# Optimization experiments

Hardware: AMD Instinct MI355X
Metric: run time of the kernel (lower is better)

The kernel has to match this reference:

```python
import jax, jax.numpy as jnp
import numpy as np

D = 768   # embedding_dimensions (richness) — hardcoded in source
H = 3     # heads — hardcoded in source


def setup_inputs() -> dict:
    key = jax.random.key(0)
    ks = jax.random.split(key, 12)
    s = 1.0 / np.sqrt(D)
    s3 = 1.0 / np.sqrt(H * D)
    return {
        "x": jax.random.normal(ks[0], (4, 2048, D), dtype=jnp.float32),
        # QKV projections: Linear(D, D*H), stored as (in, out)
        "Wq": jax.random.uniform(ks[1], (D, D * H), jnp.float32, -s, s),
        "bq": jax.random.uniform(ks[2], (D * H,), jnp.float32, -s, s),
        "Wk": jax.random.uniform(ks[3], (D, D * H), jnp.float32, -s, s),
        "bk": jax.random.uniform(ks[4], (D * H,), jnp.float32, -s, s),
        "Wv": jax.random.uniform(ks[5], (D, D * H), jnp.float32, -s, s),
        "bv": jax.random.uniform(ks[6], (D * H,), jnp.float32, -s, s),
        # final projection: Linear(H*D, D)
        "Wo": jax.random.uniform(ks[7], (H * D, D), jnp.float32, -s3, s3),
        "bo": jax.random.uniform(ks[8], (D,), jnp.float32, -s3, s3),
        # FFN: Linear(D, D) + LeakyReLU
        "Wf": jax.random.uniform(ks[9], (D, D), jnp.float32, -s, s),
        "bf": jax.random.uniform(ks[10], (D,), jnp.float32, -s, s),
    }


def reference(x, Wq, bq, Wk, bk, Wv, bv, Wo, bo, Wf, bf):
    B, S, _ = x.shape
    # QKV: [B,S,H*D] -> [B,H,S,D]  (head dim == full D, as in source)
    q = (x @ Wq + bq).reshape(B, S, H, D).transpose(0, 2, 1, 3)
    k = (x @ Wk + bk).reshape(B, S, H, D).transpose(0, 2, 1, 3)
    v = (x @ Wv + bv).reshape(B, S, H, D).transpose(0, 2, 1, 3)
    # unscaled attention scores (source applies no 1/sqrt(d))
    scores = jnp.einsum('bhqd,bhkd->bhqk', q, k)
    # faithful masking: tril of the scores themselves, fill zeros with -99999
    masked = jnp.where(jnp.tril(scores) == 0, jnp.float32(-99999.0), scores)
    attn = jax.nn.softmax(masked, axis=-1)
    o = jnp.einsum('bhqk,bhkd->bhqd', attn, v)
    o = o.transpose(0, 2, 1, 3).reshape(B, S, H * D)
    a = o @ Wo + bo
    # "normalisation": subtract global mean over the whole tensor
    n = a - jnp.mean(a)
    y = n + x  # residual
    return jax.nn.leaky_relu(y @ Wf + bf, negative_slope=0.01)
```

## Files before the change

kernel.cpp:

```cpp
#include <hip/hip_runtime.h>
#include <hip/hip_bf16.h>

typedef __attribute__((ext_vector_type(8))) __bf16 bf16x8;
typedef __attribute__((ext_vector_type(4))) float f32x4;
typedef unsigned short u16;

#define DEV static __device__ __forceinline__

#define BAR() asm volatile("s_barrier" ::: "memory")
#define VMCNT3() asm volatile("s_waitcnt vmcnt(3)" ::: "memory")
#define VMCNT0() asm volatile("s_waitcnt vmcnt(0)" ::: "memory")

DEV void load_lds16(const void* g, void* l) {
  __builtin_amdgcn_global_load_lds(
      (const __attribute__((address_space(1))) unsigned int*)g,
      (__attribute__((address_space(3))) unsigned int*)l, 16, 0, 0);
}

DEV u16 bf16bits(float v) {
  __hip_bfloat16 h = __float2bfloat16(v);
  return __builtin_bit_cast(u16, h);
}

DEV float bf2f(u16 u) {
  return __builtin_bit_cast(float, (unsigned)u << 16);
}

DEV bf16x8 rdfrag(const u16* region, int row, int ks, int l) {
  const int cb = (((ks << 6) | ((l >> 4) << 4)) ^ ((l & 7) << 4));
  return *(const bf16x8*)((const char*)region + row * 128 + cb);
}

DEV bf16x8 rdfrag32(const u16* region, int row, int l) {
  const int cb = (((l >> 4) ^ ((row >> 1) & 3)) << 4);
  return *(const bf16x8*)((const char*)region + row * 64 + cb);
}

struct OffN { unsigned long long a[12], b[12], c[12]; };

enum { G128_SC = 0, G128_PV = 1, G128_PLAIN = 2, G128_LEAKY = 3 };

__global__ __launch_bounds__(512, 1) void k_qkv256(
    const u16* __restrict__ A, const u16* __restrict__ B,
    const float* __restrict__ bias, u16* __restrict__ C, u16* __restrict__ Vt)
{
  int flat = blockIdx.y * 27 + blockIdx.x;
  flat = (flat & 7) * 108 + (flat >> 3);
  const int n0 = (flat % 27) * 256, m0 = (flat / 27) * 256;
  const int lda = 768, ldb = 768, nkt = 12;

  __shared__ u16 smem[65536];

  const int tid = threadIdx.x;
  const int l = tid & 63;
  const int wid = tid >> 6;
  const int wm = wid >> 1, wn = wid & 1;

  const int r0s = wid * 16 + (l >> 3);
  const int ces = ((l & 7) ^ (l >> 3)) << 3;
  const size_t aR0 = (size_t)(m0 + r0s) * lda + ces;
  const size_t aR1 = aR0 + (size_t)8 * lda;
  const size_t bR0 = (size_t)(n0 + r0s) * ldb + ces;
  const size_t bR1 = bR0 + (size_t)8 * ldb;
  const size_t hA = (size_t)128 * lda, hB = (size_t)128 * ldb;
  const int dst0 = wid * 1024 + l * 8, dst1 = dst0 + 512;
  u16* As0 = smem;
  u16* Bs0 = smem + 32768;

#define STAGE_A(bf, h, kkv) do {                                 \
    u16* Lp = As0 + (bf) * 16384 + (h) * 8192;                   \
    load_lds16(A + aR0 + ((h) ? hA : 0) + (kkv), Lp + dst0);     \
    load_lds16(A + aR1 + ((h) ? hA : 0) + (kkv), Lp + dst1);     \
  } while (0)
#define STAGE_B(bf, h, kkv) do {                                 \
    u16* Lp = Bs0 + (bf) * 16384 + (h) * 8192;                   \
    load_lds16(B + bR0 + ((h) ? hB : 0) + (kkv), Lp + dst0);     \
    load_lds16(B + bR1 + ((h) ? hB : 0) + (kkv), Lp + dst1);     \
  } while (0)

  f32x4 acc[2][2][2][4] = {};
  bf16x8 af[2][2], bA[4][2], bB[4][2];

#define MFMA16(QM, QN, BARR)                                                  \
    __builtin_amdgcn_s_setprio(1);                                            \
    _Pragma("unroll") for (int ks = 0; ks < 2; ks++)                          \
      _Pragma("unroll") for (int fm = 0; fm < 2; fm++)                        \
        _Pragma("unroll") for (int fn = 0; fn < 4; fn++)                      \
          acc[QM][QN][fm][fn] = __builtin_amdgcn_mfma_f32_16x16x32_bf16(      \
              af[fm][ks], BARR[fn][ks], acc[QM][QN][fm][fn], 0, 0, 0);        \
    __builtin_amdgcn_s_setprio(0);

#define RD_A(half)                                                            \
    _Pragma("unroll") for (int fm = 0; fm < 2; fm++)                          \
      _Pragma("unroll") for (int ks = 0; ks < 2; ks++)                        \
        af[fm][ks] = rdfrag(half, wm * 32 + fm * 16 + (l & 15), ks, l);
#define RD_B(dstv, half)                                                      \
    _Pragma("unroll") for (int fn = 0; fn < 4; fn++)                          \
      _Pragma("unroll") for (int ks = 0; ks < 2; ks++)                        \
        dstv[fn][ks] = rdfrag(half, wn * 64 + fn * 16 + (l & 15), ks, l);

  STAGE_A(0, 0, 0); STAGE_B(0, 0, 0); STAGE_B(0, 1, 0); STAGE_A(0, 1, 0);
  STAGE_A(1, 0, 64); STAGE_B(1, 0, 64); STAGE_B(1, 1, 64);
  VMCNT3();
  BAR();

  for (int t = 0; t < nkt; ++t) {
    const int cur = t & 1, nxt = cur ^ 1;
    const int kk1 = (t + 1) << 6, kk2 = (t + 2) << 6;
    const bool s1 = (t + 1 < nkt), s2 = (t + 2 < nkt);
    RD_A(As0 + cur * 16384);
    RD_B(bA, Bs0 + cur * 16384);
    if (s1) STAGE_A(nxt, 1, kk1);
    BAR();
    MFMA16(0, 0, bA);
    BAR();
    RD_B(bB, Bs0 + cur * 16384 + 8192);
    if (s2) STAGE_A(cur, 0, kk2);
    BAR();
    MFMA16(0, 1, bB);
    BAR();
    RD_A(As0 + cur * 16384 + 8192);
    if (s2) STAGE_B(cur, 0, kk2);
    BAR();
    MFMA16(1, 1, bB);
    BAR();
    if (s2) STAGE_B(cur, 1, kk2);
    BAR();
    MFMA16(1, 0, bA);
    if (s2) { VMCNT3(); } else { VMCNT0(); }
    BAR();
  }
#undef RD_A
#undef RD_B
#undef MFMA16
#undef STAGE_A
#undef STAGE_B

  __syncthreads();
  const int sel = n0 >= 4608 ? 2 : (n0 >= 2304 ? 1 : 0);
  const int r0c = (l >> 4) << 2;
  if (sel == 2) {
#pragma unroll
    for (int Qm = 0; Qm < 2; Qm++)
#pragma unroll
      for (int Qn = 0; Qn < 2; Qn++)
#pragma unroll
        for (int fn = 0; fn < 4; fn++) {
          const int coll = Qn * 128 + wn * 64 + fn * 16 + (l & 15);
          const float bv = bias[n0 + coll];
#pragma unroll
          for (int fm = 0; fm < 2; fm++)
#pragma unroll
            for (int r = 0; r < 4; r++) {
              const int rowl = Qm * 128 + wm * 32 + fm * 16 + r0c + r;
              smem[coll * 256 + ((((rowl >> 3) ^ (coll & 7)) << 3) | (rowl & 7))] =
                  bf16bits(acc[Qm][Qn][fm][fn][r] + bv);
            }
        }
    __syncthreads();
    const int n0v = n0 - 4608;
    const int h = n0v / 768, d0l = n0v % 768;
    const int b = m0 >> 11, sbase = m0 & 2047;
    u16* Cb = Vt + ((size_t)(b * 3 + h) * 768 + d0l) * 2048 + sbase;
#pragma unroll
    for (int j = 0; j < 16; j++) {
      const int dr = j * 16 + (tid >> 5);
      const int c8 = tid & 31;
      bf16x8 v = *(const bf16x8*)&smem[dr * 256 + ((c8 ^ (dr & 7)) << 3)];
      *(bf16x8*)&Cb[(size_t)dr * 2048 + c8 * 8] = v;
    }
  } else {
#pragma unroll
    for (int Qm = 0; Qm < 2; Qm++)
#pragma unroll
      for (int Qn = 0; Qn < 2; Qn++)
#pragma unroll
        for (int fn = 0; fn < 4; fn++) {
          const int coll = Qn * 128 + wn * 64 + fn * 16 + (l & 15);
          const float bv = bias[n0 + coll];
#pragma unroll
          for (int fm = 0; fm < 2; fm++)
#pragma unroll
            for (int r = 0; r < 4; r++) {
              const int rowl = Qm * 128 + wm * 32 + fm * 16 + r0c + r;
              smem[rowl * 256 + (coll ^ (((rowl >> 2) & 3) << 4))] =
                  bf16bits(acc[Qm][Qn][fm][fn][r] + bv);
            }
        }
    __syncthreads();
    u16* Cb = C + (size_t)sel * (8192ull * 2304) + (n0 - sel * 2304);
#pragma unroll
    for (int j = 0; j < 16; j++) {
      const int rowl = j * 16 + (tid >> 5);
      const int c = (tid & 31) * 8;
      bf16x8 v = *(const bf16x8*)&smem[rowl * 256 + (c ^ (((rowl >> 2) & 3) << 4))];
      *(bf16x8*)&Cb[(size_t)(m0 + rowl) * 2304 + c] = v;
    }
  }
}

template<int MODE>
__global__ __launch_bounds__(512, 4) void k_g128(
    const u16* __restrict__ Abase, const u16* __restrict__ Bbase,
    const float* __restrict__ bias, void* __restrict__ Cbase,
    float* __restrict__ part,
    long lda, long ldb, long ldc, int K, OffN off)
{
  int m0, n0, z, r = 0, rb = 0, nkt, arow0, brow0;
  const u16 *A, *B;
  if (MODE == G128_SC) {
    r = blockIdx.y; z = blockIdx.z;
    rb = r >> 1;
    if ((int)blockIdx.x > rb) return;
    m0 = r * 128; n0 = blockIdx.x * 256;
    nkt = K >> 5;
    A = Abase + off.a[z]; B = Bbase + off.b[z];
    arow0 = m0; brow0 = n0;
  } else if (MODE == G128_PV) {
    r = 15 - (int)blockIdx.y;
    rb = r >> 1;
    z = blockIdx.x / 3;
    m0 = r * 128; n0 = (blockIdx.x % 3) * 256;
    nkt = (rb + 1) * 8;
    lda = (long)(rb + 1) * 256;
    A = Abase + off.a[z] + (size_t)32768 * rb * (rb + 1);
    B = Bbase + off.b[z];
    arow0 = (r & 1) * 128; brow0 = n0;
  } else {
    z = 0;
    m0 = blockIdx.y * 128; n0 = blockIdx.x * 256;
    nkt = K >> 5;
    A = Abase; B = Bbase;
    arow0 = m0; brow0 = n0;
  }

  __shared__ u16 smem[36864];

  const int tid = threadIdx.x;
  const int l = tid & 63;
  const int wid = tid >> 6;
  const int wm = wid & 1;
  const int wn = wid >> 1;

  const int ces = (((tid & 3) ^ ((tid >> 3) & 3)) << 3);
  const u16* aS  = A + (size_t)(arow0 + (tid >> 2)) * lda + ces;
  const u16* bS0 = B + (size_t)(brow0 + (tid >> 2)) * ldb + ces;
  const u16* bS1 = bS0 + (size_t)128 * ldb;
  const int t8 = tid * 8;

#define STG(buf, kkv) do {                         \
    u16* Lp = smem + (buf) * 12288;                \
    load_lds16(aS + (kkv), Lp + t8);               \
    load_lds16(bS0 + (kkv), Lp + 4096 + t8);       \
    load_lds16(bS1 + (kkv), Lp + 8192 + t8);       \
  } while (0)

  f32x4 acc[4][4] = {};
  bf16x8 af[4], bf[4];

  STG(0, 0);
  STG(1, 32);
  VMCNT3();
  BAR();

  for (int t = 0; t < nkt; ++t) {
    const u16* Ar = smem + (t % 3) * 12288;
    const u16* Br = Ar + 4096;
#pragma unroll
    for (int fm = 0; fm < 4; fm++)
      af[fm] = rdfrag32(Ar, wm * 64 + fm * 16 + (l & 15), l);
#pragma unroll
    for (int fn = 0; fn < 4; fn++)
      bf[fn] = rdfrag32(Br, wn * 64 + fn * 16 + (l & 15), l);
    const bool s2 = (t + 2 < nkt);
    if (s2) STG((t + 2) % 3, (t + 2) << 5);
    __builtin_amdgcn_s_setprio(1);
#pragma unroll
    for (int fm = 0; fm < 4; fm++)
#pragma unroll
      for (int fn = 0; fn < 4; fn++)
        acc[fm][fn] = __builtin_amdgcn_mfma_f32_16x16x32_bf16(
            af[fm], bf[fn], acc[fm][fn], 0, 0, 0);
    __builtin_amdgcn_s_setprio(0);
    if (s2) { VMCNT3(); } else if (t + 1 < nkt) { VMCNT0(); }
    BAR();
  }
#undef STG

  const int r0c = (l >> 4) << 2;
  if (MODE == G128_SC) {
    float mx4[4][4], s4[4][4];
#pragma unroll
    for (int fm = 0; fm < 4; fm++)
#pragma unroll
      for (int rr = 0; rr < 4; rr++) {
        const int gi = m0 + wm * 64 + fm * 16 + r0c + rr;
        float mv = -1e30f;
#pragma unroll
        for (int fn = 0; fn < 4; fn++) {
          const int gc = n0 + wn * 64 + fn * 16 + (l & 15);
          float v = (gc <= gi) ? acc[fm][fn][rr] : -1e30f;
          acc[fm][fn][rr] = v;
          mv = fmaxf(mv, v);
        }
        mx4[fm][rr] = mv;
      }
#pragma unroll
    for (int o = 1; o < 16; o <<= 1)
#pragma unroll
      for (int fm = 0; fm < 4; fm++)
#pragma unroll
        for (int rr = 0; rr < 4; rr++)
          mx4[fm][rr] = fmaxf(mx4[fm][rr], __shfl_xor(mx4[fm][rr], o, 64));
    float* redm = (float*)smem;
    float* reds = redm + 512;
#pragma unroll
    for (int fm = 0; fm < 4; fm++)
#pragma unroll
      for (int rr = 0; rr < 4; rr++)
        if ((l & 15) == fm * 4 + rr)
          redm[(wm * 64 + fm * 16 + r0c + rr) * 4 + wn] = mx4[fm][rr];
    __syncthreads();
#pragma unroll
    for (int fm = 0; fm < 4; fm++)
#pragma unroll
      for (int rr = 0; rr < 4; rr++) {
        const int rowl = wm * 64 + fm * 16 + r0c + rr;
        f32x4 rm = *(const f32x4*)&redm[rowl * 4];
        const float tm = fmaxf(fmaxf(rm[0], rm[1]), fmaxf(rm[2], rm[3]));
        float ss = 0.f;
#pragma unroll
        for (int fn = 0; fn < 4; fn++) {
          const float e = __expf(acc[fm][fn][rr] - tm);
          acc[fm][fn][rr] = e;
          ss += e;
        }
        s4[fm][rr] = ss;
      }
#pragma unroll
    for (int o = 1; o < 16; o <<= 1)
#pragma unroll
      for (int fm = 0; fm < 4; fm++)
#pragma unroll
        for (int rr = 0; rr < 4; rr++)
          s4[fm][rr] += __shfl_xor(s4[fm][rr], o, 64);
#pragma unroll
    for (int fm = 0; fm < 4; fm++)
#pragma unroll
      for (int rr = 0; rr < 4; rr++)
        if ((l & 15) == fm * 4 + rr)
          reds[(wm * 64 + fm * 16 + r0c + rr) * 4 + wn] = s4[fm][rr];
    __syncthreads();
    if (tid < 128) {
      f32x4 rm = *(const f32x4*)&redm[tid * 4];
      f32x4 rs = *(const f32x4*)&reds[tid * 4];
      float2 pw;
      pw.x = fmaxf(fmaxf(rm[0], rm[1]), fmaxf(rm[2], rm[3]));
      pw.y = rs[0] + rs[1] + rs[2] + rs[3];
      ((float2*)part)[((size_t)z * 8 + blockIdx.x) * 2048 + m0 + tid] = pw;
    }
    __syncthreads();
#pragma unroll
    for (int fn = 0; fn < 4; fn++) {
      const int coll = wn * 64 + fn * 16 + (l & 15);
#pragma unroll
      for (int fm = 0; fm < 4; fm++)
#pragma unroll
        for (int rr = 0; rr < 4; rr++) {
          const int rowl = wm * 64 + fm * 16 + r0c + rr;
          smem[rowl * 256 + (coll ^ (((rowl >> 2) & 3) << 4))] =
              bf16bits(acc[fm][fn][rr]);
        }
    }
    __syncthreads();
    u16* Cb = (u16*)Cbase + off.c[z] + (size_t)32768 * rb * (rb + 1);
    const int W = (rb + 1) << 8;
    const int pr0 = (r & 1) * 128;
#pragma unroll
    for (int j = 0; j < 8; j++) {
      const int rowl = j * 16 + (tid >> 5);
      const int c = (tid & 31) * 8;
      bf16x8 v = *(const bf16x8*)&smem[rowl * 256 + (c ^ (((rowl >> 2) & 3) << 4))];
      *(bf16x8*)&Cb[(size_t)(pr0 + rowl) * W + n0 + c] = v;
    }
  } else if (MODE == G128_PV) {
    __syncthreads();
#pragma unroll
    for (int fn = 0; fn < 4; fn++) {
      const int coll = wn * 64 + fn * 16 + (l & 15);
#pragma unroll
      for (int fm = 0; fm < 4; fm++)
#pragma unroll
        for (int rr = 0; rr < 4; rr++) {
          const int rowl = wm * 64 + fm * 16 + r0c + rr;
          smem[rowl * 256 + (coll ^ (((rowl >> 2) & 3) << 4))] =
              bf16bits(acc[fm][fn][rr]);
        }
    }
    __syncthreads();
    u16* Cb = (u16*)Cbase + off.c[z] + n0;
#pragma unroll
    for (int j = 0; j < 8; j++) {
      const int rowl = j * 16 + (tid >> 5);
      const int c = (tid & 31) * 8;
      bf16x8 v = *(const bf16x8*)&smem[rowl * 256 + (c ^ (((rowl >> 2) & 3) << 4))];
      *(bf16x8*)&Cb[(size_t)(m0 + rowl) * 2304 + c] = v;
    }
  } else {
#pragma unroll
    for (int fn = 0; fn < 4; fn++) {
      const int col = n0 + wn * 64 + fn * 16 + (l & 15);
      const float bv = bias[col];
#pragma unroll
      for (int fm = 0; fm < 4; fm++)
#pragma unroll
        for (int rr = 0; rr < 4; rr++) {
          const int rowl = wm * 64 + fm * 16 + r0c + rr;
          float v = acc[fm][fn][rr] + bv;
          if (MODE == G128_LEAKY) v = v > 0.f ? v : 0.01f * v;
          ((float*)Cbase)[(size_t)(m0 + rowl) * ldc + col] = v;
        }
    }
  }
}

__global__ __launch_bounds__(256) void k_cast_x(const float* __restrict__ in,
                                                u16* __restrict__ out) {
  const size_t i = ((size_t)blockIdx.x * 256 + threadIdx.x) * 4;
  float4 v = *(const float4*)&in[i];
  ushort4 o;
  o.x = bf16bits(v.x); o.y = bf16bits(v.y); o.z = bf16bits(v.z); o.w = bf16bits(v.w);
  *(ushort4*)&out[i] = o;
}

__global__ __launch_bounds__(256) void k_wt(const float* __restrict__ in,
                                            u16* __restrict__ out, int R, int C) {
  __shared__ float tile[32][33];
  const int c0 = blockIdx.x * 32, r0 = blockIdx.y * 32;
  const int tx = threadIdx.x, ty = threadIdx.y;
#pragma unroll
  for (int k = 0; k < 4; k++)
    tile[ty + 8 * k][tx] = in[(size_t)(r0 + ty + 8 * k) * C + c0 + tx];
  __syncthreads();
#pragma unroll
  for (int k = 0; k < 4; k++)
    out[(size_t)(c0 + ty + 8 * k) * R + r0 + tx] = bf16bits(tile[tx][ty + 8 * k]);
}

__global__ __launch_bounds__(256) void k_bias_concat(const float* __restrict__ bq,
                                                     const float* __restrict__ bk,
                                                     const float* __restrict__ bv,
                                                     float* __restrict__ out) {
  const int i = blockIdx.x * 256 + threadIdx.x;
  if (i < 2304) out[i] = bq[i];
  else if (i < 4608) out[i] = bk[i - 2304];
  else if (i < 6912) out[i] = bv[i - 4608];
}

__global__ __launch_bounds__(256) void k_rescale(u16* __restrict__ P,
                                                 const float* __restrict__ part) {
  const int w = threadIdx.x >> 6, l = threadIdx.x & 63;
  const int gi = blockIdx.x * 4 + w;
  const int z = blockIdx.y;
  const int rb = gi >> 8;
  const int W = (rb + 1) << 8;
  const int nt = rb + 1;
  const float2* pp = (const float2*)part + (size_t)z * 16384 + gi;
  float m = -1e30f;
  for (int t = 0; t < nt; t++) m = fmaxf(m, pp[(size_t)t * 2048].x);
  float den = 0.f;
  for (int t = 0; t < nt; t++) {
    float2 q = pp[(size_t)t * 2048];
    den += q.y * __expf(q.x - m);
  }
  const float inv = 1.f / den;
  u16* Prow = P + (size_t)z * 2359296 + (size_t)32768 * rb * (rb + 1) +
              (size_t)(gi & 255) * W;
  for (int t = 0; t < nt; t++) {
    const float ft = __expf(pp[(size_t)t * 2048].x - m) * inv;
    ushort4 v = *(const ushort4*)&Prow[t * 256 + l * 4];
    v.x = bf16bits(bf2f(v.x) * ft);
    v.y = bf16bits(bf2f(v.y) * ft);
    v.z = bf16bits(bf2f(v.z) * ft);
    v.w = bf16bits(bf2f(v.w) * ft);
    *(ushort4*)&Prow[t * 256 + l * 4] = v;
  }
}

__global__ __launch_bounds__(256) void k_red1(const float* __restrict__ a,
                                              float* __restrict__ part) {
  float s = 0.f;
  for (size_t idx = (size_t)blockIdx.x * 256 + threadIdx.x; idx < 6291456ull; idx += 2048ull * 256)
    s += a[idx];
#pragma unroll
  for (int o = 32; o >= 1; o >>= 1) s += __shfl_xor(s, o, 64);
  __shared__ float r[4];
  const int t = threadIdx.x, w = t >> 6;
  if ((t & 63) == 0) r[w] = s;
  __syncthreads();
  if (t == 0) part[blockIdx.x] = r[0] + r[1] + r[2] + r[3];
}

__global__ __launch_bounds__(256) void k_red2(const float* __restrict__ part,
                                              float* __restrict__ mean) {
  const int t = threadIdx.x;
  float s = 0.f;
  for (int i = t; i < 2048; i += 256) s += part[i];
#pragma unroll
  for (int o = 32; o >= 1; o >>= 1) s += __shfl_xor(s, o, 64);
  __shared__ float r[4];
  const int w = t >> 6;
  if ((t & 63) == 0) r[w] = s;
  __syncthreads();
  if (t == 0) mean[0] = (r[0] + r[1] + r[2] + r[3]) * (1.f / 6291456.f);
}

__global__ __launch_bounds__(256) void k_residual(const float* __restrict__ a,
                                                  const float* __restrict__ x,
                                                  const float* __restrict__ meanp,
                                                  u16* __restrict__ yb) {
  const float mean = meanp[0];
  const size_t i = ((size_t)blockIdx.x * 256 + threadIdx.x) * 4;
  float4 av = *(const float4*)&a[i];
  float4 xv = *(const float4*)&x[i];
  ushort4 o;
  o.x = bf16bits(av.x - mean + xv.x);
  o.y = bf16bits(av.y - mean + xv.y);
  o.z = bf16bits(av.z - mean + xv.z);
  o.w = bf16bits(av.w - mean + xv.w);
  *(ushort4*)&yb[i] = o;
}

extern "C" void kernel_launch(void* const* d_in, const int* in_sizes, int n_in,
                              void* d_out, int out_size, void* d_ws, size_t ws_size,
                              hipStream_t stream) {
  const float* x   = (const float*)d_in[0];
  const float* Wq  = (const float*)d_in[1];
  const float* bq  = (const float*)d_in[2];
  const float* Wk  = (const float*)d_in[3];
  const float* bk  = (const float*)d_in[4];
  const float* Wv  = (const float*)d_in[5];
  const float* bv  = (const float*)d_in[6];
  const float* Wo  = (const float*)d_in[7];
  const float* bo  = (const float*)d_in[8];
  const float* Wf  = (const float*)d_in[9];
  const float* bfb = (const float*)d_in[10];

  char* ws = (char*)d_ws;
  const size_t MSZ    = 37748736;
  const size_t o_Wqkvt = 0;
  const size_t o_Wot  = 10616832;
  const size_t o_Wft  = o_Wot + 3538944;
  const size_t o_bqkv = o_Wft + 1179648;
  const size_t o_prt  = o_bqkv + 32768;
  const size_t o_mn   = o_prt + 8192;
  const size_t o_part = o_mn + 256;
  const size_t o_xb   = o_part + 1572864;
  const size_t o_Q    = o_xb + 12582912;
  const size_t o_K    = o_Q + MSZ;
  const size_t o_Vt   = o_K + MSZ;
  const size_t o_P    = o_Vt + MSZ;
  const size_t o_end  = o_P + 56623104;
  if (ws_size < o_end) return;

  const size_t o_O  = o_Q;
  const size_t o_a  = o_K;
  const size_t o_yb = o_xb;

  OffN z0{};
  dim3 b32(32, 8);

  k_cast_x<<<6144, 256, 0, stream>>>(x, (u16*)(ws + o_xb));
  k_wt<<<dim3(72, 24), b32, 0, stream>>>(Wq, (u16*)(ws + o_Wqkvt), 768, 2304);
  k_wt<<<dim3(72, 24), b32, 0, stream>>>(Wk, (u16*)(ws + o_Wqkvt) + 2304 * 768, 768, 2304);
  k_wt<<<dim3(72, 24), b32, 0, stream>>>(Wv, (u16*)(ws + o_Wqkvt) + 2 * 2304 * 768, 768, 2304);
  k_wt<<<dim3(24, 72), b32, 0, stream>>>(Wo, (u16*)(ws + o_Wot), 2304, 768);
  k_wt<<<dim3(24, 24), b32, 0, stream>>>(Wf, (u16*)(ws + o_Wft), 768, 768);
  k_bias_concat<<<27, 256, 0, stream>>>(bq, bk, bv, (float*)(ws + o_bqkv));

  k_qkv256<<<dim3(27, 32), 512, 0, stream>>>(
      (const u16*)(ws + o_xb), (const u16*)(ws + o_Wqkvt),
      (const float*)(ws + o_bqkv), (u16*)(ws + o_Q), (u16*)(ws + o_Vt));

  OffN so{}, po{};
  for (int zz = 0; zz < 12; zz++) {
    const int b = zz / 3, h = zz % 3;
    so.a[zz] = (size_t)b * 2048 * 2304 + (size_t)h * 768;
    so.b[zz] = so.a[zz];
    so.c[zz] = (size_t)zz * 2359296;
    po.a[zz] = so.c[zz];
    po.b[zz] = (size_t)zz * 768 * 2048;
    po.c[zz] = so.a[zz];
  }
  k_g128<G128_SC><<<dim3(8, 16, 12), 512, 0, stream>>>(
      (const u16*)(ws + o_Q), (const u16*)(ws + o_K), nullptr, ws + o_P,
      (float*)(ws + o_part), 2304, 2304, 0, 768, so);
  k_rescale<<<dim3(512, 12), 256, 0, stream>>>((u16*)(ws + o_P),
                                               (const float*)(ws + o_part));
  k_g128<G128_PV><<<dim3(36, 16), 512, 0, stream>>>(
      (const u16*)(ws + o_P), (const u16*)(ws + o_Vt), nullptr, ws + o_O,
      nullptr, 0, 2048, 0, 0, po);

  k_g128<G128_PLAIN><<<dim3(3, 64), 512, 0, stream>>>(
      (const u16*)(ws + o_O), (const u16*)(ws + o_Wot), bo, ws + o_a,
      nullptr, 2304, 2304, 768, 2304, z0);

  k_red1<<<2048, 256, 0, stream>>>((const float*)(ws + o_a), (float*)(ws + o_prt));
  k_red2<<<1, 256, 0, stream>>>((const float*)(ws + o_prt), (float*)(ws + o_mn));
  k_residual<<<6144, 256, 0, stream>>>((const float*)(ws + o_a), x,
                                       (const float*)(ws + o_mn), (u16*)(ws + o_yb));

  k_g128<G128_LEAKY><<<dim3(3, 64), 512, 0, stream>>>(
      (const u16*)(ws + o_yb), (const u16*)(ws + o_Wft), bfb, d_out,
      nullptr, 768, 768, 768, 768, z0);
}
```

Before: 387.4 us.

## Restructure QKV GEMM to triple-buffered K=32 pipeline and merge weight transposes

Rewrites the QKV GEMM main loop to use K-steps of 32 with a three-stage LDS ring buffer and one barrier per iteration, in place of the previous K=64 double-buffer with many interleaved barriers. LDS use drops to 96KB and launch bounds allow two blocks per CU to raise occupancy. The epilogue now writes out in two halves to fit the smaller LDS, which adds extra syncs. The three QKV weight-transpose launches are also merged into one 3D-grid launch to cut launch overhead.

```diff
diff --git a/kernel.cpp b/kernel.cpp
--- a/kernel.cpp
+++ b/kernel.cpp
@@ -8,6 +8,7 @@
 #define DEV static __device__ __forceinline__
 
 #define BAR() asm volatile("s_barrier" ::: "memory")
+#define VMCNT4() asm volatile("s_waitcnt vmcnt(4)" ::: "memory")
 #define VMCNT3() asm volatile("s_waitcnt vmcnt(3)" ::: "memory")
 #define VMCNT0() asm volatile("s_waitcnt vmcnt(0)" ::: "memory")
 
@@ -26,11 +27,6 @@
   return __builtin_bit_cast(float, (unsigned)u << 16);
 }
 
-DEV bf16x8 rdfrag(const u16* region, int row, int ks, int l) {
-  const int cb = (((ks << 6) | ((l >> 4) << 4)) ^ ((l & 7) << 4));
-  return *(const bf16x8*)((const char*)region + row * 128 + cb);
-}
-
 DEV bf16x8 rdfrag32(const u16* region, int row, int l) {
   const int cb = (((l >> 4) ^ ((row >> 1) & 3)) << 4);
   return *(const bf16x8*)((const char*)region + row * 64 + cb);
@@ -40,161 +36,131 @@
 
 enum { G128_SC = 0, G128_PV = 1, G128_PLAIN = 2, G128_LEAKY = 3 };
 
-__global__ __launch_bounds__(512, 1) void k_qkv256(
+__global__ __launch_bounds__(512, 2) void k_qkv256(
     const u16* __restrict__ A, const u16* __restrict__ B,
     const float* __restrict__ bias, u16* __restrict__ C, u16* __restrict__ Vt)
 {
   int flat = blockIdx.y * 27 + blockIdx.x;
   flat = (flat & 7) * 108 + (flat >> 3);
   const int n0 = (flat % 27) * 256, m0 = (flat / 27) * 256;
-  const int lda = 768, ldb = 768, nkt = 12;
-
-  __shared__ u16 smem[65536];
+  const int nkt = 24;
+
+  __shared__ u16 smem[49152];
 
   const int tid = threadIdx.x;
   const int l = tid & 63;
   const int wid = tid >> 6;
-  const int wm = wid >> 1, wn = wid & 1;
-
-  const int r0s = wid * 16 + (l >> 3);
-  const int ces = ((l & 7) ^ (l >> 3)) << 3;
-  const size_t aR0 = (size_t)(m0 + r0s) * lda + ces;
-  const size_t aR1 = aR0 + (size_t)8 * lda;
-  const size_t bR0 = (size_t)(n0 + r0s) * ldb + ces;
-  const size_t bR1 = bR0 + (size_t)8 * ldb;
-  const size_t hA = (size_t)128 * lda, hB = (size_t)128 * ldb;
-  const int dst0 = wid * 1024 + l * 8, dst1 = dst0 + 512;
-  u16* As0 = smem;
-  u16* Bs0 = smem + 32768;
-
-#define STAGE_A(bf, h, kkv) do {                                 \
-    u16* Lp = As0 + (bf) * 16384 + (h) * 8192;                   \
-    load_lds16(A + aR0 + ((h) ? hA : 0) + (kkv), Lp + dst0);     \
-    load_lds16(A + aR1 + ((h) ? hA : 0) + (kkv), Lp + dst1);     \
+  const int wm = wid >> 1;
+  const int wn = wid & 1;
+
+  const int ces = (((tid & 3) ^ ((tid >> 3) & 3)) << 3);
+  const u16* aS = A + (size_t)(m0 + (tid >> 2)) * 768 + ces;
+  const u16* bS = B + (size_t)(n0 + (tid >> 2)) * 768 + ces;
+  const int t8 = tid * 8;
+
+#define STG(buf, kkv) do {                               \
+    u16* Lp = smem + (buf) * 16384;                      \
+    load_lds16(aS + (kkv), Lp + t8);                     \
+    load_lds16(aS + 128 * 768 + (kkv), Lp + 4096 + t8);  \
+    load_lds16(bS + (kkv), Lp + 8192 + t8);              \
+    load_lds16(bS + 128 * 768 + (kkv), Lp + 12288 + t8); \
   } while (0)
-#define STAGE_B(bf, h, kkv) do {                                 \
-    u16* Lp = Bs0 + (bf) * 16384 + (h) * 8192;                   \
-    load_lds16(B + bR0 + ((h) ? hB : 0) + (kkv), Lp + dst0);     \
-    load_lds16(B + bR1 + ((h) ? hB : 0) + (kkv), Lp + dst1);     \
-  } while (0)
-
-  f32x4 acc[2][2][2][4] = {};
-  bf16x8 af[2][2], bA[4][2], bB[4][2];
-
-#define MFMA16(QM, QN, BARR)                                                  \
-    __builtin_amdgcn_s_setprio(1);                                            \
-    _Pragma("unroll") for (int ks = 0; ks < 2; ks++)                          \
-      _Pragma("unroll") for (int fm = 0; fm < 2; fm++)                        \
-        _Pragma("unroll") for (int fn = 0; fn < 4; fn++)                      \
-          acc[QM][QN][fm][fn] = __builtin_amdgcn_mfma_f32_16x16x32_bf16(      \
-              af[fm][ks], BARR[fn][ks], acc[QM][QN][fm][fn], 0, 0, 0);        \
+
+  f32x4 acc[4][8] = {};
+  bf16x8 af[4], bf[8];
+
+  STG(0, 0);
+  STG(1, 32);
+  VMCNT4();
+  BAR();
+
+  for (int t = 0; t < nkt; ++t) {
+    const u16* Ar = smem + (t % 3) * 16384;
+    const u16* Br = Ar + 8192;
+#pragma unroll
+    for (int fm = 0; fm < 4; fm++)
+      af[fm] = rdfrag32(Ar, wm * 64 + fm * 16 + (l & 15), l);
+#pragma unroll
+    for (int fn = 0; fn < 8; fn++)
+      bf[fn] = rdfrag32(Br, wn * 128 + fn * 16 + (l & 15), l);
+    const bool s2 = (t + 2 < nkt);
+    if (s2) STG((t + 2) % 3, (t + 2) << 5);
+    __builtin_amdgcn_s_setprio(1);
+#pragma unroll
+    for (int fm = 0; fm < 4; fm++)
+#pragma unroll
+      for (int fn = 0; fn < 8; fn++)
+        acc[fm][fn] = __builtin_amdgcn_mfma_f32_16x16x32_bf16(
+            af[fm], bf[fn], acc[fm][fn], 0, 0, 0);
     __builtin_amdgcn_s_setprio(0);
-
-#define RD_A(half)                                                            \
-    _Pragma("unroll") for (int fm = 0; fm < 2; fm++)                          \
-      _Pragma("unroll") for (int ks = 0; ks < 2; ks++)                        \
-        af[fm][ks] = rdfrag(half, wm * 32 + fm * 16 + (l & 15), ks, l);
-#define RD_B(dstv, half)                                                      \
-    _Pragma("unroll") for (int fn = 0; fn < 4; fn++)                          \
-      _Pragma("unroll") for (int ks = 0; ks < 2; ks++)                        \
-        dstv[fn][ks] = rdfrag(half, wn * 64 + fn * 16 + (l & 15), ks, l);
-
-  STAGE_A(0, 0, 0); STAGE_B(0, 0, 0); STAGE_B(0, 1, 0); STAGE_A(0, 1, 0);
-  STAGE_A(1, 0, 64); STAGE_B(1, 0, 64); STAGE_B(1, 1, 64);
-  VMCNT3();
-  BAR();
-
-  for (int t = 0; t < nkt; ++t) {
-    const int cur = t & 1, nxt = cur ^ 1;
-    const int kk1 = (t + 1) << 6, kk2 = (t + 2) << 6;
-    const bool s1 = (t + 1 < nkt), s2 = (t + 2 < nkt);
-    RD_A(As0 + cur * 16384);
-    RD_B(bA, Bs0 + cur * 16384);
-    if (s1) STAGE_A(nxt, 1, kk1);
+    if (s2) { VMCNT4(); } else if (t + 1 < nkt) { VMCNT0(); }
     BAR();
-    MFMA16(0, 0, bA);
-    BAR();
-    RD_B(bB, Bs0 + cur * 16384 + 8192);
-    if (s2) STAGE_A(cur, 0, kk2);
-    BAR();
-    MFMA16(0, 1, bB);
-    BAR();
-    RD_A(As0 + cur * 16384 + 8192);
-    if (s2) STAGE_B(cur, 0, kk2);
-    BAR();
-    MFMA16(1, 1, bB);
-    BAR();
-    if (s2) STAGE_B(cur, 1, kk2);
-    BAR();
-    MFMA16(1, 0, bA);
-    if (s2) { VMCNT3(); } else { VMCNT0(); }
-    BAR();
-  }
-#undef RD_A
-#undef RD_B
-#undef MFMA16
-#undef STAGE_A
-#undef STAGE_B
-
+  }
+#undef STG
+
+  const int r0c = (l >> 4) << 2;
+  const int sel = n0 >= 4608 ? 2 : (n0 >= 2304 ? 1 : 0);
   __syncthreads();
-  const int sel = n0 >= 4608 ? 2 : (n0 >= 2304 ? 1 : 0);
-  const int r0c = (l >> 4) << 2;
   if (sel == 2) {
-#pragma unroll
-    for (int Qm = 0; Qm < 2; Qm++)
-#pragma unroll
-      for (int Qn = 0; Qn < 2; Qn++)
-#pragma unroll
-        for (int fn = 0; fn < 4; fn++) {
-          const int coll = Qn * 128 + wn * 64 + fn * 16 + (l & 15);
+    const int n0v = n0 - 4608;
+    const int hh = n0v / 768, d0l = n0v % 768;
+    const int bb = m0 >> 11, sbase = m0 & 2047;
+    u16* Cb = Vt + ((size_t)(bb * 3 + hh) * 768 + d0l) * 2048 + sbase;
+#pragma unroll
+    for (int hc = 0; hc < 2; hc++) {
+      if (wn == hc) {
+#pragma unroll
+        for (int fn = 0; fn < 8; fn++) {
+          const int cl = fn * 16 + (l & 15);
+          const float bv = bias[n0 + hc * 128 + cl];
+#pragma unroll
+          for (int fm = 0; fm < 4; fm++)
+#pragma unroll
+            for (int rr = 0; rr < 4; rr++) {
+              const int rowl = wm * 64 + fm * 16 + r0c + rr;
+              smem[cl * 256 + ((((rowl >> 3) ^ (cl & 7)) << 3) | (rowl & 7))] =
+                  bf16bits(acc[fm][fn][rr] + bv);
+            }
+        }
+      }
+      __syncthreads();
+#pragma unroll
+      for (int j = 0; j < 8; j++) {
+        const int cl = j * 16 + (tid >> 5);
+        const int c8 = tid & 31;
+        bf16x8 v = *(const bf16x8*)&smem[cl * 256 + ((c8 ^ (cl & 7)) << 3)];
+        *(bf16x8*)&Cb[(size_t)(hc * 128 + cl) * 2048 + c8 * 8] = v;
+      }
+      __syncthreads();
+    }
+  } else {
+    u16* Cb = C + (size_t)sel * (8192ull * 2304) + (n0 - sel * 2304);
+#pragma unroll
+    for (int hf = 0; hf < 2; hf++) {
+      if ((wm >> 1) == hf) {
+#pragma unroll
+        for (int fn = 0; fn < 8; fn++) {
+          const int coll = wn * 128 + fn * 16 + (l & 15);
           const float bv = bias[n0 + coll];
 #pragma unroll
-          for (int fm = 0; fm < 2; fm++)
-#pragma unroll
-            for (int r = 0; r < 4; r++) {
-              const int rowl = Qm * 128 + wm * 32 + fm * 16 + r0c + r;
-              smem[coll * 256 + ((((rowl >> 3) ^ (coll & 7)) << 3) | (rowl & 7))] =
-                  bf16bits(acc[Qm][Qn][fm][fn][r] + bv);
+          for (int fm = 0; fm < 4; fm++)
+#pragma unroll
+            for (int rr = 0; rr < 4; rr++) {
+              const int rloc = (wm & 1) * 64 + fm * 16 + r0c + rr;
+              smem[rloc * 256 + (coll ^ (((rloc >> 2) & 3) << 4))] =
+                  bf16bits(acc[fm][fn][rr] + bv);
             }
         }
-    __syncthreads();
-    const int n0v = n0 - 4608;
-    const int h = n0v / 768, d0l = n0v % 768;
-    const int b = m0 >> 11, sbase = m0 & 2047;
-    u16* Cb = Vt + ((size_t)(b * 3 + h) * 768 + d0l) * 2048 + sbase;
-#pragma unroll
-    for (int j = 0; j < 16; j++) {
-      const int dr = j * 16 + (tid >> 5);
-      const int c8 = tid & 31;
-      bf16x8 v = *(const bf16x8*)&smem[dr * 256 + ((c8 ^ (dr & 7)) << 3)];
-      *(bf16x8*)&Cb[(size_t)dr * 2048 + c8 * 8] = v;
-    }
-  } else {
-#pragma unroll
-    for (int Qm = 0; Qm < 2; Qm++)
-#pragma unroll
-      for (int Qn = 0; Qn < 2; Qn++)
-#pragma unroll
-        for (int fn = 0; fn < 4; fn++) {
-          const int coll = Qn * 128 + wn * 64 + fn * 16 + (l & 15);
-          const float bv = bias[n0 + coll];
-#pragma unroll
-          for (int fm = 0; fm < 2; fm++)
-#pragma unroll
-            for (int r = 0; r < 4; r++) {
-              const int rowl = Qm * 128 + wm * 32 + fm * 16 + r0c + r;
-              smem[rowl * 256 + (coll ^ (((rowl >> 2) & 3) << 4))] =
-                  bf16bits(acc[Qm][Qn][fm][fn][r] + bv);
-            }
-        }
-    __syncthreads();
-    u16* Cb = C + (size_t)sel * (8192ull * 2304) + (n0 - sel * 2304);
-#pragma unroll
-    for (int j = 0; j < 16; j++) {
-      const int rowl = j * 16 + (tid >> 5);
-      const int c = (tid & 31) * 8;
-      bf16x8 v = *(const bf16x8*)&smem[rowl * 256 + (c ^ (((rowl >> 2) & 3) << 4))];
-      *(bf16x8*)&Cb[(size_t)(m0 + rowl) * 2304 + c] = v;
+      }
+      __syncthreads();
+#pragma unroll
+      for (int j = 0; j < 8; j++) {
+        const int rowl = j * 16 + (tid >> 5);
+        const int c = (tid & 31) * 8;
+        bf16x8 v = *(const bf16x8*)&smem[rowl * 256 + (c ^ (((rowl >> 2) & 3) << 4))];
+        *(bf16x8*)&Cb[(size_t)(m0 + hf * 128 + rowl) * 2304 + c] = v;
+      }
+      __syncthreads();
     }
   }
 }
@@ -433,6 +399,24 @@
   *(ushort4*)&out[i] = o;
 }
 
+__global__ __launch_bounds__(256) void k_wt3(const float* __restrict__ w0,
+                                             const float* __restrict__ w1,
+                                             const float* __restrict__ w2,
+                                             u16* __restrict__ out) {
+  const float* in = blockIdx.z == 0 ? w0 : (blockIdx.z == 1 ? w1 : w2);
+  u16* o = out + (size_t)blockIdx.z * 2304 * 768;
+  __shared__ float tile[32][33];
+  const int c0 = blockIdx.x * 32, r0 = blockIdx.y * 32;
+  const int tx = threadIdx.x, ty = threadIdx.y;
+#pragma unroll
+  for (int k = 0; k < 4; k++)
+    tile[ty + 8 * k][tx] = in[(size_t)(r0 + ty + 8 * k) * 2304 + c0 + tx];
+  __syncthreads();
+#pragma unroll
+  for (int k = 0; k < 4; k++)
+    o[(size_t)(c0 + ty + 8 * k) * 768 + r0 + tx] = bf16bits(tile[tx][ty + 8 * k]);
+}
+
 __global__ __launch_bounds__(256) void k_wt(const float* __restrict__ in,
                                             u16* __restrict__ out, int R, int C) {
   __shared__ float tile[32][33];
@@ -571,9 +555,7 @@
   dim3 b32(32, 8);
 
   k_cast_x<<<6144, 256, 0, stream>>>(x, (u16*)(ws + o_xb));
-  k_wt<<<dim3(72, 24), b32, 0, stream>>>(Wq, (u16*)(ws + o_Wqkvt), 768, 2304);
-  k_wt<<<dim3(72, 24), b32, 0, stream>>>(Wk, (u16*)(ws + o_Wqkvt) + 2304 * 768, 768, 2304);
-  k_wt<<<dim3(72, 24), b32, 0, stream>>>(Wv, (u16*)(ws + o_Wqkvt) + 2 * 2304 * 768, 768, 2304);
+  k_wt3<<<dim3(72, 24, 3), b32, 0, stream>>>(Wq, Wk, Wv, (u16*)(ws + o_Wqkvt));
   k_wt<<<dim3(24, 72), b32, 0, stream>>>(Wo, (u16*)(ws + o_Wot), 2304, 768);
   k_wt<<<dim3(24, 24), b32, 0, stream>>>(Wf, (u16*)(ws + o_Wft), 768, 768);
   k_bias_concat<<<27, 256, 0, stream>>>(bq, bk, bv, (float*)(ws + o_bqkv));
```

Measured after the change: 392.1 us. About the same (+1.2%).

## Fuse softmax rescale into PV GEMM and merge QKV weight transposes

Applied to the files above, without the earlier changes.

Removes the standalone k_rescale pass, which read and rewrote the whole bf16 probability matrix. Instead, the PV kernel computes per-row, per-block exp factors and the inverse denominator into an LDS table. It scales the A fragments in registers before each MFMA and applies 1/den in the epilogue. The three Q/K/V weight transposes now run as one launch, and the QKV GEMM's vmcnt wait is relaxed from 3 to 6 outstanding loads. The trade is extra VALU work and LDS reads inside the PV main loop. The looser vmcnt wait risks reading staged data before it has landed.

```diff
diff --git a/kernel.cpp b/kernel.cpp
--- a/kernel.cpp
+++ b/kernel.cpp
@@ -8,6 +8,8 @@
 #define DEV static __device__ __forceinline__
 
 #define BAR() asm volatile("s_barrier" ::: "memory")
+#define LGKM0() asm volatile("s_waitcnt lgkmcnt(0)" ::: "memory")
+#define VMCNT6() asm volatile("s_waitcnt vmcnt(6)" ::: "memory")
 #define VMCNT3() asm volatile("s_waitcnt vmcnt(3)" ::: "memory")
 #define VMCNT0() asm volatile("s_waitcnt vmcnt(0)" ::: "memory")
 
@@ -20,10 +22,6 @@
 DEV u16 bf16bits(float v) {
   __hip_bfloat16 h = __float2bfloat16(v);
   return __builtin_bit_cast(u16, h);
-}
-
-DEV float bf2f(u16 u) {
-  return __builtin_bit_cast(float, (unsigned)u << 16);
 }
 
 DEV bf16x8 rdfrag(const u16* region, int row, int ks, int l) {
@@ -101,7 +99,7 @@
 
   STAGE_A(0, 0, 0); STAGE_B(0, 0, 0); STAGE_B(0, 1, 0); STAGE_A(0, 1, 0);
   STAGE_A(1, 0, 64); STAGE_B(1, 0, 64); STAGE_B(1, 1, 64);
-  VMCNT3();
+  VMCNT6();
   BAR();
 
   for (int t = 0; t < nkt; ++t) {
@@ -127,7 +125,7 @@
     if (s2) STAGE_B(cur, 1, kk2);
     BAR();
     MFMA16(1, 0, bA);
-    if (s2) { VMCNT3(); } else { VMCNT0(); }
+    if (s2) { VMCNT6(); } else { VMCNT0(); }
     BAR();
   }
 #undef RD_A
@@ -234,7 +232,7 @@
     arow0 = m0; brow0 = n0;
   }
 
-  __shared__ u16 smem[36864];
+  __shared__ u16 smem[39168];
 
   const int tid = threadIdx.x;
   const int l = tid & 63;
@@ -255,6 +253,24 @@
     load_lds16(bS1 + (kkv), Lp + 8192 + t8);       \
   } while (0)
 
+  float* ftab = (float*)(smem + 36864);
+  if (MODE == G128_PV) {
+    if (tid < 128) {
+      const float2* pp = (const float2*)part + (size_t)z * 16384 + (m0 + tid);
+      float m = -1e30f;
+      for (int t = 0; t <= rb; t++) m = fmaxf(m, pp[(size_t)t * 2048].x);
+      float den = 0.f;
+      for (int t = 0; t <= rb; t++) {
+        const float2 q = pp[(size_t)t * 2048];
+        const float e = __expf(q.x - m);
+        den += q.y * e;
+        ftab[tid * 9 + t] = e;
+      }
+      ftab[tid * 9 + 8] = 1.f / den;
+    }
+    LGKM0();
+  }
+
   f32x4 acc[4][4] = {};
   bf16x8 af[4], bf[4];
 
@@ -272,6 +288,17 @@
 #pragma unroll
     for (int fn = 0; fn < 4; fn++)
       bf[fn] = rdfrag32(Br, wn * 64 + fn * 16 + (l & 15), l);
+    if (MODE == G128_PV) {
+      const int tcol = t >> 3;
+#pragma unroll
+      for (int fm = 0; fm < 4; fm++) {
+        const int row = wm * 64 + fm * 16 + (l & 15);
+        const float ft = ftab[row * 9 + tcol];
+#pragma unroll
+        for (int i = 0; i < 8; i++)
+          af[fm][i] = (__bf16)((float)af[fm][i] * ft);
+      }
+    }
     const bool s2 = (t + 2 < nkt);
     if (s2) STG((t + 2) % 3, (t + 2) << 5);
     __builtin_amdgcn_s_setprio(1);
@@ -394,7 +421,7 @@
         for (int rr = 0; rr < 4; rr++) {
           const int rowl = wm * 64 + fm * 16 + r0c + rr;
           smem[rowl * 256 + (coll ^ (((rowl >> 2) & 3) << 4))] =
-              bf16bits(acc[fm][fn][rr]);
+              bf16bits(acc[fm][fn][rr] * ftab[rowl * 9 + 8]);
         }
     }
     __syncthreads();
@@ -431,6 +458,24 @@
   ushort4 o;
   o.x = bf16bits(v.x); o.y = bf16bits(v.y); o.z = bf16bits(v.z); o.w = bf16bits(v.w);
   *(ushort4*)&out[i] = o;
+}
+
+__global__ __launch_bounds__(256) void k_wt3(const float* __restrict__ w0,
+                                             const float* __restrict__ w1,
+                                             const float* __restrict__ w2,
+                                             u16* __restrict__ out) {
+  const float* in = blockIdx.z == 0 ? w0 : (blockIdx.z == 1 ? w1 : w2);
+  u16* o = out + (size_t)blockIdx.z * 2304 * 768;
+  __shared__ float tile[32][33];
+  const int c0 = blockIdx.x * 32, r0 = blockIdx.y * 32;
+  const int tx = threadIdx.x, ty = threadIdx.y;
+#pragma unroll
+  for (int k = 0; k < 4; k++)
+    tile[ty + 8 * k][tx] = in[(size_t)(r0 + ty + 8 * k) * 2304 + c0 + tx];
+  __syncthreads();
+#pragma unroll
+  for (int k = 0; k < 4; k++)
+    o[(size_t)(c0 + ty + 8 * k) * 768 + r0 + tx] = bf16bits(tile[tx][ty + 8 * k]);
 }
 
 __global__ __launch_bounds__(256) void k_wt(const float* __restrict__ in,
@@ -455,36 +500,6 @@
   if (i < 2304) out[i] = bq[i];
   else if (i < 4608) out[i] = bk[i - 2304];
   else if (i < 6912) out[i] = bv[i - 4608];
-}
-
-__global__ __launch_bounds__(256) void k_rescale(u16* __restrict__ P,
-                                                 const float* __restrict__ part) {
-  const int w = threadIdx.x >> 6, l = threadIdx.x & 63;
-  const int gi = blockIdx.x * 4 + w;
-  const int z = blockIdx.y;
-  const int rb = gi >> 8;
-  const int W = (rb + 1) << 8;
-  const int nt = rb + 1;
-  const float2* pp = (const float2*)part + (size_t)z * 16384 + gi;
-  float m = -1e30f;
-  for (int t = 0; t < nt; t++) m = fmaxf(m, pp[(size_t)t * 2048].x);
-  float den = 0.f;
-  for (int t = 0; t < nt; t++) {
-    float2 q = pp[(size_t)t * 2048];
-    den += q.y * __expf(q.x - m);
-  }
-  const float inv = 1.f / den;
-  u16* Prow = P + (size_t)z * 2359296 + (size_t)32768 * rb * (rb + 1) +
-              (size_t)(gi & 255) * W;
-  for (int t = 0; t < nt; t++) {
-    const float ft = __expf(pp[(size_t)t * 2048].x - m) * inv;
-    ushort4 v = *(const ushort4*)&Prow[t * 256 + l * 4];
-    v.x = bf16bits(bf2f(v.x) * ft);
-    v.y = bf16bits(bf2f(v.y) * ft);
-    v.z = bf16bits(bf2f(v.z) * ft);
-    v.w = bf16bits(bf2f(v.w) * ft);
-    *(ushort4*)&Prow[t * 256 + l * 4] = v;
-  }
 }
 
 __global__ __launch_bounds__(256) void k_red1(const float* __restrict__ a,
@@ -571,9 +586,7 @@
   dim3 b32(32, 8);
 
   k_cast_x<<<6144, 256, 0, stream>>>(x, (u16*)(ws + o_xb));
-  k_wt<<<dim3(72, 24), b32, 0, stream>>>(Wq, (u16*)(ws + o_Wqkvt), 768, 2304);
-  k_wt<<<dim3(72, 24), b32, 0, stream>>>(Wk, (u16*)(ws + o_Wqkvt) + 2304 * 768, 768, 2304);
-  k_wt<<<dim3(72, 24), b32, 0, stream>>>(Wv, (u16*)(ws + o_Wqkvt) + 2 * 2304 * 768, 768, 2304);
+  k_wt3<<<dim3(72, 24, 3), b32, 0, stream>>>(Wq, Wk, Wv, (u16*)(ws + o_Wqkvt));
   k_wt<<<dim3(24, 72), b32, 0, stream>>>(Wo, (u16*)(ws + o_Wot), 2304, 768);
   k_wt<<<dim3(24, 24), b32, 0, stream>>>(Wf, (u16*)(ws + o_Wft), 768, 768);
   k_bias_concat<<<27, 256, 0, stream>>>(bq, bk, bv, (float*)(ws + o_bqkv));
@@ -595,11 +608,9 @@
   k_g128<G128_SC><<<dim3(8, 16, 12), 512, 0, stream>>>(
       (const u16*)(ws + o_Q), (const u16*)(ws + o_K), nullptr, ws + o_P,
       (float*)(ws + o_part), 2304, 2304, 0, 768, so);
-  k_rescale<<<dim3(512, 12), 256, 0, stream>>>((u16*)(ws + o_P),
-                                               (const float*)(ws + o_part));
   k_g128<G128_PV><<<dim3(36, 16), 512, 0, stream>>>(
       (const u16*)(ws + o_P), (const u16*)(ws + o_Vt), nullptr, ws + o_O,
-      nullptr, 0, 2048, 0, 0, po);
+      (float*)(ws + o_part), 0, 2048, 0, 0, po);
 
   k_g128<G128_PLAIN><<<dim3(3, 64), 512, 0, stream>>>(
       (const u16*)(ws + o_O), (const u16*)(ws + o_Wot), bo, ws + o_a,
```

After: 374.7 us. -3.3%, faster.
